# Kernel tuning notes

Hardware: AMD Instinct MI355X
Metric: run time of the kernel (lower is better)

The kernel has to match this reference:

```python
import jax, jax.numpy as jnp
import numpy as np

N = 30000        # nodes
E_EDGES = 960000 # edges (avg degree 32)
G = 16           # graphs in batch
D_IN, D_H, D_OUT = 6, 256, 256
L = 3            # GraphConv layers per expert
N_EXP, TOP_K = 8, 2


def _lin(key, fan_in, shape):
    return jax.random.normal(key, shape, dtype=jnp.float32) / np.sqrt(fan_in)


def setup_inputs() -> dict:
    key = jax.random.key(0)
    ks = jax.random.split(key, 12)
    x = jax.random.normal(ks[0], (N, D_IN), dtype=jnp.float32)
    edge_index = jax.random.randint(ks[1], (2, E_EDGES), 0, N, dtype=jnp.int64)
    batch = jnp.sort(jax.random.randint(ks[2], (N,), 0, G, dtype=jnp.int64))
    return {
        "x": x,
        "edge_index": edge_index,
        "batch": batch,
        # SharedBusEncoder: Linear(in, hidden) + ReLU
        "enc_W": _lin(ks[3], D_IN, (D_IN, D_H)),
        "enc_b": jnp.zeros((D_H,), jnp.float32),
        # BaseRouter: Linear(hidden+2, hidden) -> ReLU -> Linear(hidden, n_experts)
        "r_W1": _lin(ks[4], D_H + 2, (D_H + 2, D_H)),
        "r_b1": jnp.zeros((D_H,), jnp.float32),
        "r_W2": _lin(ks[5], D_H, (D_H, N_EXP)),
        "r_b2": jnp.zeros((N_EXP,), jnp.float32),
        # GraphConvExpert: L layers of PyG GraphConv (lin_rel on aggregated
        # neighbors + lin_root on self), stacked over [layer, expert].
        "Wrel": _lin(ks[6], D_H, (L, N_EXP, D_H, D_OUT)),
        "brel": jnp.zeros((L, N_EXP, D_OUT), jnp.float32),
        "Wroot": _lin(ks[7], D_H, (L, N_EXP, D_H, D_OUT)),
    }


def _forward(x, edge_index, batch, enc_W, enc_b, r_W1, r_b1, r_W2, r_b2,
             Wrel, brel, Wroot):
    src, dst = edge_index[0], edge_index[1]
    # encoder
    h = jax.nn.relu(x @ enc_W + enc_b)  # [N, D_H]

    # graph size features: per-node [log(#nodes), log(#edges)] of its graph
    n_g = jax.ops.segment_sum(jnp.ones((N,), jnp.float32), batch, num_segments=G)
    e_g = jax.ops.segment_sum(jnp.ones((E_EDGES,), jnp.float32), batch[src], num_segments=G)
    size = jnp.log(jnp.maximum(jnp.stack([n_g, e_g], axis=-1), 1.0))  # [G, 2]
    size_feat = size[batch]  # [N, 2]

    # router + sparse top-k routing
    r_h = jax.nn.relu(jnp.concatenate([h, size_feat], axis=-1) @ r_W1 + r_b1)
    logits = r_h @ r_W2 + r_b2            # [N, E]
    probs = jax.nn.softmax(logits, axis=-1)
    vals, idx = jax.lax.top_k(probs, TOP_K)
    vals = vals / jnp.sum(vals, axis=-1, keepdims=True)
    sparse = jnp.zeros((N, N_EXP), probs.dtype).at[
        jnp.arange(N)[:, None], idx].set(vals)  # [N, E]

    # all-expert GraphConv stacks (dense over experts, as in the original)
    agg0 = jax.ops.segment_sum(h[src], dst, num_segments=N)  # [N, D_H]
    H = jnp.einsum('nd,edf->enf', agg0, Wrel[0]) + brel[0][:, None, :] \
        + jnp.einsum('nd,edf->enf', h, Wroot[0])             # [E, N, D]
    for l in range(1, L):
        H = jax.nn.relu(H)
        A = jax.vmap(lambda hh: jax.ops.segment_sum(hh[src], dst, num_segments=N))(H)
        H = jnp.einsum('end,edf->enf', A, Wrel[l]) + brel[l][:, None, :] \
            + jnp.einsum('end,edf->enf', H, Wroot[l])

    # mask-and-sum combine
    return jnp.einsum('enf,ne->nf', H, sparse)  # [N, D_OUT]


def reference(x, edge_index, batch, enc_W, enc_b, r_W1, r_b1, r_W2, r_b2,
              Wrel, brel, Wroot):
    return _forward(x, edge_index, batch, enc_W, enc_b, r_W1, r_b1, r_W2,
                    r_b2, Wrel, brel, Wroot)
```

## Files before the change

kernel.cpp:

```cpp
#include <hip/hip_runtime.h>
#include <hip/hip_bf16.h>
#include <math.h>

#define NEXP 8
#define GNUM 16
#define DH 256

typedef __attribute__((ext_vector_type(8))) short s16x8;
typedef __attribute__((ext_vector_type(4))) float f32x4;
typedef unsigned short u16;
typedef unsigned int u32;

__device__ __forceinline__ float bitsToF(u32 b){ union{u32 u; float f;} c; c.u=b; return c.f; }
__device__ __forceinline__ u16 f2bf(float f){
  union{float f; u32 u;} c; c.f=f;
  u32 r = c.u + 0x7fffu + ((c.u>>16)&1u);
  return (u16)(r>>16);
}

#define GLOAD_LDS16(gp, lp) __builtin_amdgcn_global_load_lds( \
    (const __attribute__((address_space(1))) unsigned int*)(gp), \
    (__attribute__((address_space(3))) unsigned int*)(lp), 16, 0, 0)

__global__ void count_edges_k(const int* __restrict__ ei, const int* __restrict__ batch,
                              int* __restrict__ deg, int* __restrict__ eg, int E){
  __shared__ int leg[GNUM];
  int t = threadIdx.x;
  if (t < GNUM) leg[t] = 0;
  __syncthreads();
  int i = blockIdx.x*blockDim.x + t;
  if (i < E){
    int s = ei[i];
    int d = ei[E + i];
    atomicAdd(&deg[d], 1);
    atomicAdd(&leg[batch[s]], 1);
  }
  __syncthreads();
  if (t < GNUM){ int v = leg[t]; if (v) atomicAdd(&eg[t], v); }
}

__global__ void count_nodes_k(const int* __restrict__ batch, int* __restrict__ ng, int N){
  __shared__ int lng[GNUM];
  int t = threadIdx.x;
  if (t < GNUM) lng[t] = 0;
  __syncthreads();
  int i = blockIdx.x*blockDim.x + t;
  if (i < N) atomicAdd(&lng[batch[i]], 1);
  __syncthreads();
  if (t < GNUM){ int v = lng[t]; if (v) atomicAdd(&ng[t], v); }
}

#define SCAN_T 1024
#define SCAN_CH 32
__global__ __launch_bounds__(1024) void scan_deg_k(const int* __restrict__ deg,
    int* __restrict__ row_ptr, int* __restrict__ cursor, int N){
  __shared__ int part[SCAN_T];
  int t = threadIdx.x;
  int base = t*SCAN_CH;
  int loc[SCAN_CH];
  int s = 0;
  #pragma unroll
  for (int j=0;j<SCAN_CH;j++){
    int i = base+j;
    int v = (i<N)? deg[i] : 0;
    loc[j] = s; s += v;
  }
  part[t] = s;
  __syncthreads();
  for (int off=1; off<SCAN_T; off<<=1){
    int add = (t>=off)? part[t-off] : 0;
    __syncthreads();
    part[t] += add;
    __syncthreads();
  }
  int ex = (t==0)? 0 : part[t-1];
  #pragma unroll
  for (int j=0;j<SCAN_CH;j++){
    int i = base+j;
    if (i<N){ int v = ex + loc[j]; row_ptr[i]=v; cursor[i]=v; }
  }
  if (t == SCAN_T-1) row_ptr[N] = part[SCAN_T-1];
}

__global__ void scatter_edges_k(const int* __restrict__ ei, int* __restrict__ cursor,
                                int* __restrict__ csr_src, int E){
  int i = blockIdx.x*blockDim.x + threadIdx.x;
  if (i>=E) return;
  int s = ei[i];
  int d = ei[E + i];
  int pos = atomicAdd(&cursor[d], 1);
  csr_src[pos] = s;
}

__global__ void size_feats_k(const int* __restrict__ ng, const int* __restrict__ eg,
                             float* __restrict__ sizef){
  int g = threadIdx.x;
  if (g < GNUM){
    sizef[g*2]   = logf(fmaxf((float)ng[g], 1.f));
    sizef[g*2+1] = logf(fmaxf((float)eg[g], 1.f));
  }
}

__global__ void mark_fail_k(float* out){ out[0] = __builtin_nanf(""); }

__global__ __launch_bounds__(256) void encoder_k(const float* __restrict__ x,
    const float* __restrict__ W, const float* __restrict__ b,
    float* __restrict__ hf, u16* __restrict__ bh, int N){
  int n = blockIdx.x; if (n>=N) return;
  int f = threadIdx.x;
  float acc = b[f];
  #pragma unroll
  for (int k=0;k<6;k++) acc += x[n*6+k]*W[k*DH+f];
  acc = fmaxf(acc, 0.f);
  hf[(size_t)n*DH+f] = acc;
  bh[(size_t)n*DH+f] = f2bf(acc);
}

__global__ __launch_bounds__(256) void convw_k(const float* __restrict__ Wrel,
    const float* __restrict__ Wroot, u16* __restrict__ WT){
  __shared__ float tile[64][65];
  int tx = threadIdx.x;
  int ty = threadIdx.y;
  int kt = blockIdx.x & 3, ct = blockIdx.x >> 2;
  int srcRoot = blockIdx.y;
  int le = blockIdx.z;
  const float* src = (srcRoot ? Wroot : Wrel) + (size_t)le*65536;
  #pragma unroll
  for (int i=0;i<16;i++){
    int kl = ty + i*4;
    tile[kl][tx] = src[(size_t)(kt*64 + kl)*256 + ct*64 + tx];
  }
  __syncthreads();
  u16* dst = WT + (size_t)le*131072 + (srcRoot ? 256 : 0) + kt*64;
  #pragma unroll
  for (int i=0;i<16;i++){
    int cl = ty + i*4;
    dst[(size_t)(ct*64 + cl)*512 + tx] = f2bf(tile[tx][cl]);
  }
}

#define R1N 32
__global__ __launch_bounds__(256) void router1_k(
    const float* __restrict__ hf, const float* __restrict__ sizef,
    const int* __restrict__ batch,
    const float* __restrict__ W1, const float* __restrict__ b1,
    float* __restrict__ rh, int N)
{
  __shared__ float xin[R1N][264];
  int t = threadIdx.x;
  int lane = t & 63, w = t >> 6;
  int n0 = blockIdx.x * R1N;
  #pragma unroll
  for (int i=0;i<R1N;i++){
    int n = n0 + i;
    xin[i][t] = (n<N) ? hf[(size_t)n*DH + t] : 0.f;
  }
  if (t < R1N){
    int n = n0 + t;
    int g = (n<N) ? (int)batch[n] : 0;
    xin[t][256] = sizef[g*2];
    xin[t][257] = sizef[g*2+1];
    xin[t][258] = 0.f; xin[t][259] = 0.f;
    xin[t][260] = 0.f; xin[t][261] = 0.f; xin[t][262] = 0.f; xin[t][263] = 0.f;
  }
  __syncthreads();

  int wn = w*8;
  float bb[4];
  #pragma unroll
  for (int c=0;c<4;c++) bb[c] = b1[lane + c*64];
  float acc[8][4];
  #pragma unroll
  for (int i=0;i<8;i++)
    #pragma unroll
    for (int c=0;c<4;c++) acc[i][c] = bb[c];

  #pragma unroll 2
  for (int k4=0; k4<256; k4+=4){
    float w4[4][4];
    #pragma unroll
    for (int j=0;j<4;j++)
      #pragma unroll
      for (int c=0;c<4;c++)
        w4[j][c] = W1[(size_t)(k4+j)*DH + lane + c*64];
    #pragma unroll
    for (int i=0;i<8;i++){
      f32x4 xv = *(const f32x4*)&xin[wn+i][k4];
      #pragma unroll
      for (int j=0;j<4;j++)
        #pragma unroll
        for (int c=0;c<4;c++)
          acc[i][c] += xv[j]*w4[j][c];
    }
  }
  float w256[4], w257[4];
  #pragma unroll
  for (int c=0;c<4;c++){
    w256[c] = W1[(size_t)256*DH + lane + c*64];
    w257[c] = W1[(size_t)257*DH + lane + c*64];
  }
  #pragma unroll
  for (int i=0;i<8;i++){
    float s0 = xin[wn+i][256], s1 = xin[wn+i][257];
    #pragma unroll
    for (int c=0;c<4;c++) acc[i][c] += s0*w256[c] + s1*w257[c];
  }
  #pragma unroll
  for (int i=0;i<8;i++){
    int n = n0 + wn + i;
    if (n < N){
      #pragma unroll
      for (int c=0;c<4;c++)
        rh[(size_t)n*DH + lane + c*64] = fmaxf(acc[i][c], 0.f);
    }
  }
}

__global__ __launch_bounds__(256) void router2_k(
    const float* __restrict__ rh, const float* __restrict__ W2,
    const float* __restrict__ b2,
    int* __restrict__ ridx, float* __restrict__ rval, int N)
{
  __shared__ float w2s[NEXP][260];
  int t = threadIdx.x;
  for (int i=t; i<NEXP*DH; i+=256){
    int e = i >> 8, k = i & 255;
    w2s[e][k] = W2[(size_t)k*NEXP + e];
  }
  __syncthreads();
  int lane = t & 63, w = t >> 6;
  int n = blockIdx.x*4 + w;
  if (n >= N) return;
  const float* r = rh + (size_t)n*DH;
  float p[NEXP];
  #pragma unroll
  for (int e=0;e<NEXP;e++) p[e] = 0.f;
  #pragma unroll
  for (int c=0;c<4;c++){
    int k = lane + c*64;
    float rv = r[k];
    #pragma unroll
    for (int e=0;e<NEXP;e++) p[e] += rv * w2s[e][k];
  }
  #pragma unroll
  for (int off=1; off<64; off<<=1){
    #pragma unroll
    for (int e=0;e<NEXP;e++) p[e] += __shfl_xor(p[e], off, 64);
  }
  if (lane == 0){
    float l0[NEXP];
    #pragma unroll
    for (int e=0;e<NEXP;e++) l0[e] = p[e] + b2[e];
    float m = l0[0];
    #pragma unroll
    for (int e=1;e<NEXP;e++) m = fmaxf(m, l0[e]);
    float ex[NEXP];
    #pragma unroll
    for (int e=0;e<NEXP;e++) ex[e] = expf(l0[e]-m);
    int e0=0; float b0v=ex[0];
    #pragma unroll
    for (int e=1;e<NEXP;e++) if (ex[e]>b0v){b0v=ex[e]; e0=e;}
    int e1=(e0==0)?1:0; float b1v=ex[e1];
    #pragma unroll
    for (int e=0;e<NEXP;e++) if (e!=e0 && ex[e]>b1v){b1v=ex[e]; e1=e;}
    float sv = b0v + b1v;
    rval[n*2]   = b0v/sv;
    rval[n*2+1] = b1v/sv;
    ridx[n*2]   = e0;
    ridx[n*2+1] = e1;
  }
}

__global__ __launch_bounds__(256) void rsort_k(const int* __restrict__ ridx,
    int* __restrict__ cnt, int* __restrict__ plist, int* __restrict__ ppos, int N){
  __shared__ int lcnt[NEXP];
  __shared__ int lbase[NEXP];
  int t = threadIdx.x;
  int n = blockIdx.x*256 + t;
  if (t < NEXP) lcnt[t] = 0;
  __syncthreads();
  int e0=0, e1=0, o0=0, o1=0;
  if (n < N){
    e0 = ridx[n*2];
    e1 = ridx[n*2+1];
    o0 = atomicAdd(&lcnt[e0], 1);
    o1 = atomicAdd(&lcnt[e1], 1);
  }
  __syncthreads();
  if (t < NEXP) lbase[t] = atomicAdd(&cnt[t], lcnt[t]);
  __syncthreads();
  if (n < N){
    int p0 = lbase[e0] + o0;
    int p1 = lbase[e1] + o1;
    plist[(size_t)e0*N + p0] = n;
    plist[(size_t)e1*N + p1] = n;
    ppos[n*2]   = p0;
    ppos[n*2+1] = p1;
  }
}

__device__ __forceinline__ void agg_row(const u16* __restrict__ H,
    u16* __restrict__ Arow, const int* __restrict__ row_ptr,
    const int* __restrict__ csr_src, int node, int lane){
  int beg = row_ptr[node], end = row_ptr[node+1];
  float a0=0.f,a1=0.f,a2=0.f,a3=0.f;
  const u16* Hl = H + (lane<<2);
  int i = beg;
  for (; i+8<=end; i+=8){
    int sarr[8];
    #pragma unroll
    for (int u=0;u<8;u++) sarr[u] = csr_src[i+u];
    #pragma unroll
    for (int u=0;u<8;u++){
      uint2 v = *(const uint2*)(Hl + ((size_t)sarr[u]<<8));
      a0 += bitsToF(v.x<<16);
      a1 += bitsToF(v.x & 0xffff0000u);
      a2 += bitsToF(v.y<<16);
      a3 += bitsToF(v.y & 0xffff0000u);
    }
  }
  for (; i<end; ++i){
    int s = csr_src[i];
    uint2 v = *(const uint2*)(Hl + ((size_t)s<<8));
    a0 += bitsToF(v.x<<16);
    a1 += bitsToF(v.x & 0xffff0000u);
    a2 += bitsToF(v.y<<16);
    a3 += bitsToF(v.y & 0xffff0000u);
  }
  uint2 o;
  o.x = ((u32)f2bf(a1)<<16) | f2bf(a0);
  o.y = ((u32)f2bf(a3)<<16) | f2bf(a2);
  *(uint2*)(Arow + (lane<<2)) = o;
}

__global__ __launch_bounds__(256) void agg0_k(const u16* __restrict__ H,
    u16* __restrict__ A, const int* __restrict__ row_ptr,
    const int* __restrict__ csr_src, int N){
  int node = blockIdx.x*4 + (threadIdx.x>>6);
  if (node >= N) return;
  int lane = threadIdx.x & 63;
  agg_row(H, A + ((size_t)node<<8), row_ptr, csr_src, node, lane);
}

__device__ __forceinline__ void agg1_body(const u16* __restrict__ Hsrc,
    u16* __restrict__ Aout, const int* __restrict__ row_ptr,
    const int* __restrict__ csr_src, int N, int base, int cntN,
    int ezMask, int ezShift){
  int bid = blockIdx.x;
  int el = bid & ezMask;
  int xb = bid >> ezShift;
  int node = base + xb*4 + (threadIdx.x>>6);
  if (node >= base + cntN) return;
  int lane = threadIdx.x & 63;
  size_t NS = (size_t)N*DH;
  agg_row(Hsrc + (size_t)el*NS, Aout + (size_t)el*NS + ((size_t)node<<8),
          row_ptr, csr_src, node, lane);
}
__global__ __launch_bounds__(256) void agg1a_k(const u16* __restrict__ Hsrc,
    u16* __restrict__ Aout, const int* __restrict__ row_ptr,
    const int* __restrict__ csr_src, int N, int base, int cntN,
    int ezMask, int ezShift){
  agg1_body(Hsrc, Aout, row_ptr, csr_src, N, base, cntN, ezMask, ezShift);
}
__global__ __launch_bounds__(256) void agg1b_k(const u16* __restrict__ Hsrc,
    u16* __restrict__ Aout, const int* __restrict__ row_ptr,
    const int* __restrict__ csr_src, int N, int base, int cntN,
    int ezMask, int ezShift){
  agg1_body(Hsrc, Aout, row_ptr, csr_src, N, base, cntN, ezMask, ezShift);
}

__global__ __launch_bounds__(256) void agg2sg_k(const u16* __restrict__ Hsrc,
    u16* __restrict__ Aout, u16* __restrict__ Rout,
    const int* __restrict__ row_ptr, const int* __restrict__ csr_src,
    const int* __restrict__ plist, const int* __restrict__ cnt,
    int N, int gBase){
  int el = blockIdx.y;
  int idx = blockIdx.x*4 + (threadIdx.x>>6);
  if (idx >= cnt[gBase + el]) return;
  int node = plist[(size_t)(gBase + el)*N + idx];
  size_t NS = (size_t)N*DH;
  const u16* H = Hsrc + (size_t)el*NS;
  int lane = threadIdx.x & 63;
  uint2 rootv = *(const uint2*)(H + ((size_t)node<<8) + (lane<<2));
  agg_row(H, Aout + (size_t)el*NS + ((size_t)idx<<8), row_ptr, csr_src, node, lane);
  *(uint2*)(Rout + (size_t)el*NS + ((size_t)idx<<8) + (lane<<2)) = rootv;
}

__device__ __forceinline__ void gemm_bk64_body(
    const u16* __restrict__ aBase, const u16* __restrict__ rBase,
    const u16* __restrict__ wBase, const float* __restrict__ be,
    u16* __restrict__ Oe, int N, int relu_flag, u16* As, u16* Bs)
{
  int tid = threadIdx.x;
  int lane = tid & 63, w = tid >> 6;
  int wr = w >> 1, wc = w & 1;
  int m0 = blockIdx.x * 128;
  int n0 = blockIdx.y * 128;

  int lr8 = lane >> 3;
  int p   = (lane & 7) ^ lr8;
  long long asrc[4]; u16* aL[4];
  long long bsrc[4]; u16* bL[4];
  #pragma unroll
  for (int j=0;j<4;j++){
    int c = w*4 + j;
    int arow = m0 + c*8 + lr8; if (arow >= N) arow = N-1;
    asrc[j] = (long long)arow*256 + p*8;
    aL[j] = As + (size_t)c*512;
    int bcol = n0 + c*8 + lr8;
    bsrc[j] = (long long)bcol*512 + p*8;
    bL[j] = Bs + (size_t)c*512;
  }

  f32x4 acc[4][4];
  #pragma unroll
  for (int a=0;a<4;a++)
    #pragma unroll
    for (int b=0;b<4;b++) acc[a][b] = (f32x4){0.f,0.f,0.f,0.f};

  int fr = lane & 15;
  int fkq = lane >> 4;

  #pragma unroll 1
  for (int kk=0; kk<8; ++kk){
    const u16* sA = (kk < 4) ? aBase : rBase;
    int koff = (kk & 3) * 64;
    #pragma unroll
    for (int j=0;j<4;j++){
      GLOAD_LDS16(sA + asrc[j] + koff, aL[j]);
      GLOAD_LDS16(wBase + bsrc[j] + kk*64, bL[j]);
    }
    __syncthreads();
    #pragma unroll
    for (int kin=0; kin<2; ++kin){
      unsigned fb = (unsigned)(fkq*16 + kin*64);
      s16x8 af[4], bf[4];
      #pragma unroll
      for (int mi=0;mi<4;mi++){
        int row = wr*64 + mi*16 + fr;
        unsigned byte = ((unsigned)row << 7) + (fb ^ (((unsigned)(row & 7)) << 4));
        af[mi] = *(const s16x8*)((const char*)As + byte);
      }
      #pragma unroll
      for (int ni=0;ni<4;ni++){
        int col = wc*64 + ni*16 + fr;
        unsigned byte = ((unsigned)col << 7) + (fb ^ (((unsigned)(col & 7)) << 4));
        bf[ni] = *(const s16x8*)((const char*)Bs + byte);
      }
      #pragma unroll
      for (int mi=0;mi<4;mi++)
        #pragma unroll
        for (int ni=0;ni<4;ni++)
          acc[mi][ni] = __builtin_amdgcn_mfma_f32_16x16x32_bf16(af[mi], bf[ni], acc[mi][ni], 0, 0, 0);
    }
    __syncthreads();
  }

  int fq = lane >> 4;
  #pragma unroll
  for (int ni=0;ni<4;ni++){
    int col = n0 + wc*64 + ni*16 + fr;
    float bv = be[col];
    #pragma unroll
    for (int mi=0;mi<4;mi++){
      int rowb = m0 + wr*64 + mi*16 + fq*4;
      f32x4 v = acc[mi][ni];
      #pragma unroll
      for (int j=0;j<4;j++){
        int row = rowb + j;
        if (row < N){
          float o = v[j] + bv;
          if (relu_flag) o = fmaxf(o, 0.f);
          Oe[(size_t)row*DH + col] = f2bf(o);
        }
      }
    }
  }
}

__global__ __launch_bounds__(256,2) void gemm0g_k(
    const u16* __restrict__ A0, const u16* __restrict__ bh,
    const u16* __restrict__ WT, const float* __restrict__ bias,
    u16* __restrict__ Hout, int N){
  __shared__ u16 As[128*64];
  __shared__ u16 Bs[128*64];
  int el = blockIdx.z;
  gemm_bk64_body(A0, bh, WT + (size_t)el*(256*512), bias + el*256,
                 Hout + (size_t)el*((size_t)N*DH), N, 1, As, Bs);
}
__global__ __launch_bounds__(256,2) void gemm1g_k(
    const u16* __restrict__ Aagg, const u16* __restrict__ Hroot,
    const u16* __restrict__ WT, const float* __restrict__ bias,
    u16* __restrict__ Hout, int N){
  __shared__ u16 As[128*64];
  __shared__ u16 Bs[128*64];
  int el = blockIdx.z;
  size_t NS = (size_t)N*DH;
  gemm_bk64_body(Aagg + (size_t)el*NS, Hroot + (size_t)el*NS,
                 WT + (size_t)el*(256*512), bias + el*256,
                 Hout + (size_t)el*NS, N, 1, As, Bs);
}

__global__ __launch_bounds__(256,2) void gemm2sg_k(
    const u16* __restrict__ Aagg, const u16* __restrict__ Rc,
    const u16* __restrict__ WT, const float* __restrict__ bias,
    u16* __restrict__ Hout, const int* __restrict__ cnte, int N, int gBase)
{
  __shared__ u16 As[128*32];
  __shared__ u16 Bs[128*32];
  int el = blockIdx.z;
  int cnt = cnte[gBase + el];
  int m0 = blockIdx.x * 128;
  if (m0 >= cnt) return;
  size_t NS = (size_t)N*DH;
  const u16* aBase = Aagg + (size_t)el*NS;
  const u16* rBase = Rc + (size_t)el*NS;
  const u16* wBase = WT + (size_t)el*(256*512);
  const float* be  = bias + el*256;
  u16* Oe = Hout + (size_t)el*NS;

  int tid = threadIdx.x;
  int lane = tid & 63, w = tid >> 6;
  int wr = w >> 1, wc = w & 1;
  int n0 = blockIdx.y * 128;

  int lrow = lane >> 2;
  int q8   = (((lane & 3) ^ ((lane >> 3) & 3))) * 8;
  int r0 = w*16 + lrow;
  int r1 = (w+4)*16 + lrow;
  int ai0 = m0 + r0; if (ai0 >= cnt) ai0 = cnt-1;
  int ai1 = m0 + r1; if (ai1 >= cnt) ai1 = cnt-1;
  long long aoff0 = (long long)ai0*256 + q8;
  long long aoff1 = (long long)ai1*256 + q8;
  long long boff0 = (long long)(n0 + r0)*512 + q8;
  long long boff1 = (long long)(n0 + r1)*512 + q8;
  u16* aL0 = As + (size_t)w*512;
  u16* aL1 = As + (size_t)(w+4)*512;
  u16* bL0 = Bs + (size_t)w*512;
  u16* bL1 = Bs + (size_t)(w+4)*512;

  f32x4 acc[4][4];
  #pragma unroll
  for (int a=0;a<4;a++)
    #pragma unroll
    for (int b=0;b<4;b++) acc[a][b] = (f32x4){0.f,0.f,0.f,0.f};

  int fr = lane & 15;
  int fk = (((lane >> 4) ^ ((fr >> 1) & 3))) * 8;
  const u16* aRead = As + (size_t)(wr*64 + fr)*32 + fk;
  const u16* bRead = Bs + (size_t)(wc*64 + fr)*32 + fk;

  #pragma unroll 1
  for (int half=0; half<2; ++half){
    const u16* sA = half ? rBase : aBase;
    #pragma unroll 1
    for (int kk=0; kk<8; ++kk){
      int kin = kk*32;
      int kg  = half*256 + kin;
      GLOAD_LDS16(sA + aoff0 + kin, aL0);
      GLOAD_LDS16(sA + aoff1 + kin, aL1);
      GLOAD_LDS16(wBase + boff0 + kg, bL0);
      GLOAD_LDS16(wBase + boff1 + kg, bL1);
      __syncthreads();
      s16x8 af[4], bf[4];
      #pragma unroll
      for (int mi=0;mi<4;mi++) af[mi] = *(const s16x8*)(aRead + mi*16*32);
      #pragma unroll
      for (int ni=0;ni<4;ni++) bf[ni] = *(const s16x8*)(bRead + ni*16*32);
      #pragma unroll
      for (int mi=0;mi<4;mi++)
        #pragma unroll
        for (int ni=0;ni<4;ni++)
          acc[mi][ni] = __builtin_amdgcn_mfma_f32_16x16x32_bf16(af[mi], bf[ni], acc[mi][ni], 0, 0, 0);
      __syncthreads();
    }
  }
  int fq = lane >> 4;
  #pragma unroll
  for (int ni=0;ni<4;ni++){
    int col = n0 + wc*64 + ni*16 + fr;
    float bv = be[col];
    #pragma unroll
    for (int mi=0;mi<4;mi++){
      int rowb = m0 + wr*64 + mi*16 + fq*4;
      f32x4 v = acc[mi][ni];
      #pragma unroll
      for (int j=0;j<4;j++){
        int row = rowb + j;
        if (row < cnt){
          float o = v[j] + bv;
          Oe[(size_t)row*DH + col] = f2bf(o);
        }
      }
    }
  }
}

__global__ __launch_bounds__(256) void combine_spg_k(const u16* __restrict__ H3c,
    const int* __restrict__ ridx, const int* __restrict__ ppos,
    const float* __restrict__ rval, float* __restrict__ out,
    int N, int gBase, int ezCnt, int first){
  int n = blockIdx.x; if (n>=N) return;
  int f = threadIdx.x;
  size_t NS = (size_t)N*DH;
  size_t off = (size_t)n*DH + f;
  float acc = first ? 0.f : out[off];
  #pragma unroll
  for (int p=0;p<2;p++){
    int el = ridx[n*2+p] - gBase;
    if (el >= 0 && el < ezCnt)
      acc += rval[n*2+p] * bitsToF(((u32)H3c[(size_t)el*NS + (size_t)ppos[n*2+p]*DH + f])<<16);
  }
  out[off] = acc;
}

extern "C" void kernel_launch(void* const* d_in, const int* in_sizes, int n_in,
                              void* d_out, int out_size, void* d_ws, size_t ws_size,
                              hipStream_t stream)
{
  const float* x    = (const float*)d_in[0];
  const int*   ei   = (const int*)d_in[1];
  const int*   batch= (const int*)d_in[2];
  const float* encW = (const float*)d_in[3];
  const float* encb = (const float*)d_in[4];
  const float* rW1  = (const float*)d_in[5];
  const float* rb1  = (const float*)d_in[6];
  const float* rW2  = (const float*)d_in[7];
  const float* rb2  = (const float*)d_in[8];
  const float* Wrel = (const float*)d_in[9];
  const float* brel = (const float*)d_in[10];
  const float* Wroot= (const float*)d_in[11];
  int N = in_sizes[2];
  int E = in_sizes[1]/2;
  float* out = (float*)d_out;
  (void)n_in; (void)out_size;

  size_t NS = (size_t)N*DH;
  char* p = (char*)d_ws;
  auto carve = [&](size_t bytes)->char*{
    char* r = p; p += (bytes + 255) & ~(size_t)255; return r;
  };
  u16*  bh   = (u16*)carve(NS*2);
  u16*  WT   = (u16*)carve((size_t)3*NEXP*256*512*2);
  int*  deg  = (int*)carve((size_t)N*4 + 64*4);
  int*  ng   = deg + N;
  int*  eg   = ng + GNUM;
  int*  row_ptr = (int*)carve(((size_t)N+1)*4);
  int*  cursor  = (int*)carve((size_t)N*4);
  int*  csr     = (int*)carve((size_t)E*4);
  float* sizef  = (float*)carve(GNUM*2*4);
  int*  ridx    = (int*)carve((size_t)N*2*4);
  float* rvalv  = (float*)carve((size_t)N*2*4);
  int*  ecnt    = (int*)carve(NEXP*4);
  int*  plist   = (int*)carve((size_t)NEXP*N*4);
  int*  ppos    = (int*)carve((size_t)N*2*4);
  u16*  A0      = (u16*)carve(NS*2);
  size_t baseUsed = (size_t)(p - (char*)d_ws);

  int EZ = 0;
  for (int cand = NEXP; cand >= 1; cand >>= 1){
    if (baseUsed + (size_t)cand*3*NS*2 <= ws_size){ EZ = cand; break; }
  }
  if (EZ == 0){ mark_fail_k<<<1,1,0,stream>>>(out); return; }
  int ezShift = (EZ==8)?3 : (EZ==4)?2 : (EZ==2)?1 : 0;

  u16* Abuf = (u16*)carve((size_t)EZ*NS*2);
  u16* Hc   = (u16*)carve((size_t)EZ*NS*2);
  u16* Hn   = (u16*)carve((size_t)EZ*NS*2);
  float* hf; float* rh;
  if (EZ >= 2){ hf = (float*)Abuf; rh = (float*)Hn; }
  else {
    hf = (float*)carve(NS*4);
    rh = (float*)carve(NS*4);
    if ((size_t)(p - (char*)d_ws) > ws_size){ mark_fail_k<<<1,1,0,stream>>>(out); return; }
  }

  hipMemsetAsync(deg, 0, (size_t)N*4 + (size_t)2*GNUM*4, stream);
  hipMemsetAsync(ecnt, 0, NEXP*4, stream);

  int eb = (E + 255)/256;
  count_edges_k<<<eb, 256, 0, stream>>>(ei, batch, deg, eg, E);
  count_nodes_k<<<(N+255)/256, 256, 0, stream>>>(batch, ng, N);
  scan_deg_k<<<1, SCAN_T, 0, stream>>>(deg, row_ptr, cursor, N);
  scatter_edges_k<<<eb, 256, 0, stream>>>(ei, cursor, csr, E);
  size_feats_k<<<1, 64, 0, stream>>>(ng, eg, sizef);
  encoder_k<<<N, 256, 0, stream>>>(x, encW, encb, hf, bh, N);
  convw_k<<<dim3(16,2,3*NEXP), dim3(64,4), 0, stream>>>(Wrel, Wroot, WT);
  router1_k<<<(N+R1N-1)/R1N, 256, 0, stream>>>(hf, sizef, batch, rW1, rb1, rh, N);
  router2_k<<<(N+3)/4, 256, 0, stream>>>(rh, rW2, rb2, ridx, rvalv, N);
  rsort_k<<<(N+255)/256, 256, 0, stream>>>(ridx, ecnt, plist, ppos, N);

  int aggx = (N+3)/4;
  int mt128 = (N+127)/128;
  const size_t WE = (size_t)256*512;

  agg0_k<<<aggx, 256, 0, stream>>>(bh, A0, row_ptr, csr, N);

  int half0 = (((N+1)/2) + 3) & ~3;
  if (half0 > N) half0 = N;
  int half1 = N - half0;
  int g1a = ((half0+3)/4)*EZ;
  int g1b = ((half1+3)/4)*EZ;

  for (int g = 0; g < NEXP; g += EZ){
    gemm0g_k<<<dim3(mt128,2,EZ), 256, 0, stream>>>(A0, bh,
        WT + ((size_t)0*NEXP + g)*WE, brel + (0*NEXP + g)*256, Hc, N);
    agg1a_k<<<g1a, 256, 0, stream>>>(Hc, Abuf, row_ptr, csr, N, 0, half0, EZ-1, ezShift);
    if (half1 > 0)
      agg1b_k<<<g1b, 256, 0, stream>>>(Hc, Abuf, row_ptr, csr, N, half0, half1, EZ-1, ezShift);
    gemm1g_k<<<dim3(mt128,2,EZ), 256, 0, stream>>>(Abuf, Hc,
        WT + ((size_t)1*NEXP + g)*WE, brel + (1*NEXP + g)*256, Hn, N);
    agg2sg_k<<<dim3(aggx,EZ), 256, 0, stream>>>(Hn, Abuf, Hc, row_ptr, csr,
        plist, ecnt, N, g);
    gemm2sg_k<<<dim3(mt128,2,EZ), 256, 0, stream>>>(Abuf, Hc,
        WT + ((size_t)2*NEXP + g)*WE, brel + (2*NEXP + g)*256, Hn, ecnt, N, g);
    combine_spg_k<<<N, 256, 0, stream>>>(Hn, ridx, ppos, rvalv, out, N, g, EZ, g==0);
  }
}
```

Baseline: 1.295 ms.

## Interleave layer-0 expert outputs per node so the first aggregation gathers contiguous rows

The layer-0 GEMM now writes its output interleaved as [node, expert, feature] instead of expert-major. The first-layer aggregation becomes a single kernel with one block per node and one wave per expert. Each neighbour's data for all experts is therefore one contiguous chunk, and the CSR indices are read once and shared across experts. The GEMM body gains row-stride parameters so layer 0 can write, and layer 1 can read, the strided root operand, at the cost of strided stores and loads in those GEMMs and larger blocks (up to 512 threads) in the aggregation.

```diff
diff --git a/kernel.cpp b/kernel.cpp
--- a/kernel.cpp
+++ b/kernel.cpp
@@ -342,31 +342,44 @@
   agg_row(H, A + ((size_t)node<<8), row_ptr, csr_src, node, lane);
 }
 
-__device__ __forceinline__ void agg1_body(const u16* __restrict__ Hsrc,
+__global__ void agg1i_k(const u16* __restrict__ Hi,
     u16* __restrict__ Aout, const int* __restrict__ row_ptr,
-    const int* __restrict__ csr_src, int N, int base, int cntN,
-    int ezMask, int ezShift){
-  int bid = blockIdx.x;
-  int el = bid & ezMask;
-  int xb = bid >> ezShift;
-  int node = base + xb*4 + (threadIdx.x>>6);
-  if (node >= base + cntN) return;
+    const int* __restrict__ csr_src, int N, int EZ){
+  int node = blockIdx.x;
+  if (node >= N) return;
+  int el = threadIdx.x >> 6;
   int lane = threadIdx.x & 63;
   size_t NS = (size_t)N*DH;
-  agg_row(Hsrc + (size_t)el*NS, Aout + (size_t)el*NS + ((size_t)node<<8),
-          row_ptr, csr_src, node, lane);
-}
-__global__ __launch_bounds__(256) void agg1a_k(const u16* __restrict__ Hsrc,
-    u16* __restrict__ Aout, const int* __restrict__ row_ptr,
-    const int* __restrict__ csr_src, int N, int base, int cntN,
-    int ezMask, int ezShift){
-  agg1_body(Hsrc, Aout, row_ptr, csr_src, N, base, cntN, ezMask, ezShift);
-}
-__global__ __launch_bounds__(256) void agg1b_k(const u16* __restrict__ Hsrc,
-    u16* __restrict__ Aout, const int* __restrict__ row_ptr,
-    const int* __restrict__ csr_src, int N, int base, int cntN,
-    int ezMask, int ezShift){
-  agg1_body(Hsrc, Aout, row_ptr, csr_src, N, base, cntN, ezMask, ezShift);
+  const u16* Hl = Hi + (size_t)el*DH + (lane<<2);
+  int beg = row_ptr[node], end = row_ptr[node+1];
+  float a0=0.f,a1=0.f,a2=0.f,a3=0.f;
+  int strideSh = (EZ==8)?11 : (EZ==4)?10 : (EZ==2)?9 : 8;
+  int i = beg;
+  for (; i+8<=end; i+=8){
+    int sarr[8];
+    #pragma unroll
+    for (int u=0;u<8;u++) sarr[u] = csr_src[i+u];
+    #pragma unroll
+    for (int u=0;u<8;u++){
+      uint2 v = *(const uint2*)(Hl + ((size_t)sarr[u]<<strideSh));
+      a0 += bitsToF(v.x<<16);
+      a1 += bitsToF(v.x & 0xffff0000u);
+      a2 += bitsToF(v.y<<16);
+      a3 += bitsToF(v.y & 0xffff0000u);
+    }
+  }
+  for (; i<end; ++i){
+    int s = csr_src[i];
+    uint2 v = *(const uint2*)(Hl + ((size_t)s<<strideSh));
+    a0 += bitsToF(v.x<<16);
+    a1 += bitsToF(v.x & 0xffff0000u);
+    a2 += bitsToF(v.y<<16);
+    a3 += bitsToF(v.y & 0xffff0000u);
+  }
+  uint2 o;
+  o.x = ((u32)f2bf(a1)<<16) | f2bf(a0);
+  o.y = ((u32)f2bf(a3)<<16) | f2bf(a2);
+  *(uint2*)(Aout + (size_t)el*NS + ((size_t)node<<8) + (lane<<2)) = o;
 }
 
 __global__ __launch_bounds__(256) void agg2sg_k(const u16* __restrict__ Hsrc,
@@ -388,8 +401,10 @@
 
 __device__ __forceinline__ void gemm_bk64_body(
     const u16* __restrict__ aBase, const u16* __restrict__ rBase,
+    long long rstrideElems,
     const u16* __restrict__ wBase, const float* __restrict__ be,
-    u16* __restrict__ Oe, int N, int relu_flag, u16* As, u16* Bs)
+    u16* __restrict__ Oe, long long ostrideElems,
+    int N, int relu_flag, u16* As, u16* Bs)
 {
   int tid = threadIdx.x;
   int lane = tid & 63, w = tid >> 6;
@@ -399,13 +414,14 @@
 
   int lr8 = lane >> 3;
   int p   = (lane & 7) ^ lr8;
-  long long asrc[4]; u16* aL[4];
+  long long asrc[4]; long long rsrc[4]; u16* aL[4];
   long long bsrc[4]; u16* bL[4];
   #pragma unroll
   for (int j=0;j<4;j++){
     int c = w*4 + j;
     int arow = m0 + c*8 + lr8; if (arow >= N) arow = N-1;
     asrc[j] = (long long)arow*256 + p*8;
+    rsrc[j] = (long long)arow*rstrideElems + p*8;
     aL[j] = As + (size_t)c*512;
     int bcol = n0 + c*8 + lr8;
     bsrc[j] = (long long)bcol*512 + p*8;
@@ -423,11 +439,12 @@
 
   #pragma unroll 1
   for (int kk=0; kk<8; ++kk){
-    const u16* sA = (kk < 4) ? aBase : rBase;
+    int useRoot = (kk >= 4);
     int koff = (kk & 3) * 64;
     #pragma unroll
     for (int j=0;j<4;j++){
-      GLOAD_LDS16(sA + asrc[j] + koff, aL[j]);
+      if (useRoot) GLOAD_LDS16(rBase + rsrc[j] + koff, aL[j]);
+      else         GLOAD_LDS16(aBase + asrc[j] + koff, aL[j]);
       GLOAD_LDS16(wBase + bsrc[j] + kk*64, bL[j]);
     }
     __syncthreads();
@@ -471,7 +488,7 @@
         if (row < N){
           float o = v[j] + bv;
           if (relu_flag) o = fmaxf(o, 0.f);
-          Oe[(size_t)row*DH + col] = f2bf(o);
+          Oe[(size_t)row*ostrideElems + col] = f2bf(o);
         }
       }
     }
@@ -481,24 +498,25 @@
 __global__ __launch_bounds__(256,2) void gemm0g_k(
     const u16* __restrict__ A0, const u16* __restrict__ bh,
     const u16* __restrict__ WT, const float* __restrict__ bias,
-    u16* __restrict__ Hout, int N){
+    u16* __restrict__ Hi, int N, int EZ){
   __shared__ u16 As[128*64];
   __shared__ u16 Bs[128*64];
   int el = blockIdx.z;
-  gemm_bk64_body(A0, bh, WT + (size_t)el*(256*512), bias + el*256,
-                 Hout + (size_t)el*((size_t)N*DH), N, 1, As, Bs);
+  gemm_bk64_body(A0, bh, 256,
+                 WT + (size_t)el*(256*512), bias + el*256,
+                 Hi + (size_t)el*DH, (long long)EZ*DH, N, 1, As, Bs);
 }
 __global__ __launch_bounds__(256,2) void gemm1g_k(
-    const u16* __restrict__ Aagg, const u16* __restrict__ Hroot,
+    const u16* __restrict__ Aagg, const u16* __restrict__ Hi,
     const u16* __restrict__ WT, const float* __restrict__ bias,
-    u16* __restrict__ Hout, int N){
+    u16* __restrict__ Hout, int N, int EZ){
   __shared__ u16 As[128*64];
   __shared__ u16 Bs[128*64];
   int el = blockIdx.z;
   size_t NS = (size_t)N*DH;
-  gemm_bk64_body(Aagg + (size_t)el*NS, Hroot + (size_t)el*NS,
+  gemm_bk64_body(Aagg + (size_t)el*NS, Hi + (size_t)el*DH, (long long)EZ*DH,
                  WT + (size_t)el*(256*512), bias + el*256,
-                 Hout + (size_t)el*NS, N, 1, As, Bs);
+                 Hout + (size_t)el*NS, 256, N, 1, As, Bs);
 }
 
 __global__ __launch_bounds__(256,2) void gemm2sg_k(
@@ -662,7 +680,6 @@
     if (baseUsed + (size_t)cand*3*NS*2 <= ws_size){ EZ = cand; break; }
   }
   if (EZ == 0){ mark_fail_k<<<1,1,0,stream>>>(out); return; }
-  int ezShift = (EZ==8)?3 : (EZ==4)?2 : (EZ==2)?1 : 0;
 
   u16* Abuf = (u16*)carve((size_t)EZ*NS*2);
   u16* Hc   = (u16*)carve((size_t)EZ*NS*2);
@@ -696,20 +713,12 @@
 
   agg0_k<<<aggx, 256, 0, stream>>>(bh, A0, row_ptr, csr, N);
 
-  int half0 = (((N+1)/2) + 3) & ~3;
-  if (half0 > N) half0 = N;
-  int half1 = N - half0;
-  int g1a = ((half0+3)/4)*EZ;
-  int g1b = ((half1+3)/4)*EZ;
-
   for (int g = 0; g < NEXP; g += EZ){
     gemm0g_k<<<dim3(mt128,2,EZ), 256, 0, stream>>>(A0, bh,
-        WT + ((size_t)0*NEXP + g)*WE, brel + (0*NEXP + g)*256, Hc, N);
-    agg1a_k<<<g1a, 256, 0, stream>>>(Hc, Abuf, row_ptr, csr, N, 0, half0, EZ-1, ezShift);
-    if (half1 > 0)
-      agg1b_k<<<g1b, 256, 0, stream>>>(Hc, Abuf, row_ptr, csr, N, half0, half1, EZ-1, ezShift);
+        WT + ((size_t)0*NEXP + g)*WE, brel + (0*NEXP + g)*256, Hc, N, EZ);
+    agg1i_k<<<N, 64*EZ, 0, stream>>>(Hc, Abuf, row_ptr, csr, N, EZ);
     gemm1g_k<<<dim3(mt128,2,EZ), 256, 0, stream>>>(Abuf, Hc,
-        WT + ((size_t)1*NEXP + g)*WE, brel + (1*NEXP + g)*256, Hn, N);
+        WT + ((size_t)1*NEXP + g)*WE, brel + (1*NEXP + g)*256, Hn, N, EZ);
     agg2sg_k<<<dim3(aggx,EZ), 256, 0, stream>>>(Hn, Abuf, Hc, row_ptr, csr,
         plist, ecnt, N, g);
     gemm2sg_k<<<dim3(mt128,2,EZ), 256, 0, stream>>>(Abuf, Hc,
```

New measurement: 1.385 ms. 6.9% more time.

## Split neighbor aggregation into feature-quarter passes with 4-way edge parallelism

Applied to the files above, without the earlier changes.

The layer-1 and layer-2 aggregation kernels now process one 64-column quarter of the 256-wide feature row per launch, running four launches in turn. Within a wave, 16 lanes cover the quarter's columns and 4 lane groups take different edges, then combine through cross-lane shuffles. The aim is to shrink the gathered working set per pass so it stays in cache, and to put more independent gathers in flight per wave. In exchange there are four times as many launches, the CSR indices are re-read once per quarter, and shuffle reductions are added; the agg1 two-half split is removed.

```diff
diff --git a/kernel.cpp b/kernel.cpp
--- a/kernel.cpp
+++ b/kernel.cpp
@@ -342,48 +342,90 @@
   agg_row(H, A + ((size_t)node<<8), row_ptr, csr_src, node, lane);
 }
 
-__device__ __forceinline__ void agg1_body(const u16* __restrict__ Hsrc,
+
+__global__ __launch_bounds__(256) void agg1q_k(const u16* __restrict__ Hsrc,
     u16* __restrict__ Aout, const int* __restrict__ row_ptr,
-    const int* __restrict__ csr_src, int N, int base, int cntN,
-    int ezMask, int ezShift){
+    const int* __restrict__ csr_src, int N, int qoff, int ezMask, int ezShift){
   int bid = blockIdx.x;
   int el = bid & ezMask;
   int xb = bid >> ezShift;
-  int node = base + xb*4 + (threadIdx.x>>6);
-  if (node >= base + cntN) return;
+  int node = xb*4 + (threadIdx.x>>6);
+  if (node >= N) return;
   int lane = threadIdx.x & 63;
+  int e4 = lane >> 4, c16 = lane & 15;
   size_t NS = (size_t)N*DH;
-  agg_row(Hsrc + (size_t)el*NS, Aout + (size_t)el*NS + ((size_t)node<<8),
-          row_ptr, csr_src, node, lane);
-}
-__global__ __launch_bounds__(256) void agg1a_k(const u16* __restrict__ Hsrc,
-    u16* __restrict__ Aout, const int* __restrict__ row_ptr,
-    const int* __restrict__ csr_src, int N, int base, int cntN,
-    int ezMask, int ezShift){
-  agg1_body(Hsrc, Aout, row_ptr, csr_src, N, base, cntN, ezMask, ezShift);
-}
-__global__ __launch_bounds__(256) void agg1b_k(const u16* __restrict__ Hsrc,
-    u16* __restrict__ Aout, const int* __restrict__ row_ptr,
-    const int* __restrict__ csr_src, int N, int base, int cntN,
-    int ezMask, int ezShift){
-  agg1_body(Hsrc, Aout, row_ptr, csr_src, N, base, cntN, ezMask, ezShift);
-}
-
-__global__ __launch_bounds__(256) void agg2sg_k(const u16* __restrict__ Hsrc,
+  const u16* Hq = Hsrc + (size_t)el*NS + qoff + (c16<<2);
+  int beg = row_ptr[node], end = row_ptr[node+1];
+  float a0=0.f,a1=0.f,a2=0.f,a3=0.f;
+  for (int i = beg; i < end; i += 4){
+    int ii = i + e4;
+    if (ii < end){
+      int s = csr_src[ii];
+      uint2 v = *(const uint2*)(Hq + ((size_t)s<<8));
+      a0 += bitsToF(v.x<<16);
+      a1 += bitsToF(v.x & 0xffff0000u);
+      a2 += bitsToF(v.y<<16);
+      a3 += bitsToF(v.y & 0xffff0000u);
+    }
+  }
+  #pragma unroll
+  for (int off=16; off<64; off<<=1){
+    a0 += __shfl_xor(a0, off, 64);
+    a1 += __shfl_xor(a1, off, 64);
+    a2 += __shfl_xor(a2, off, 64);
+    a3 += __shfl_xor(a3, off, 64);
+  }
+  if (e4 == 0){
+    uint2 o;
+    o.x = ((u32)f2bf(a1)<<16) | f2bf(a0);
+    o.y = ((u32)f2bf(a3)<<16) | f2bf(a2);
+    *(uint2*)(Aout + (size_t)el*NS + ((size_t)node<<8) + qoff + (c16<<2)) = o;
+  }
+}
+
+__global__ __launch_bounds__(256) void agg2q_k(const u16* __restrict__ Hsrc,
     u16* __restrict__ Aout, u16* __restrict__ Rout,
     const int* __restrict__ row_ptr, const int* __restrict__ csr_src,
     const int* __restrict__ plist, const int* __restrict__ cnt,
-    int N, int gBase){
-  int el = blockIdx.y;
-  int idx = blockIdx.x*4 + (threadIdx.x>>6);
+    int N, int gBase, int qoff, int ezMask, int ezShift){
+  int bid = blockIdx.x;
+  int el = bid & ezMask;
+  int xb = bid >> ezShift;
+  int idx = xb*4 + (threadIdx.x>>6);
   if (idx >= cnt[gBase + el]) return;
   int node = plist[(size_t)(gBase + el)*N + idx];
+  int lane = threadIdx.x & 63;
+  int e4 = lane >> 4, c16 = lane & 15;
   size_t NS = (size_t)N*DH;
-  const u16* H = Hsrc + (size_t)el*NS;
-  int lane = threadIdx.x & 63;
-  uint2 rootv = *(const uint2*)(H + ((size_t)node<<8) + (lane<<2));
-  agg_row(H, Aout + (size_t)el*NS + ((size_t)idx<<8), row_ptr, csr_src, node, lane);
-  *(uint2*)(Rout + (size_t)el*NS + ((size_t)idx<<8) + (lane<<2)) = rootv;
+  const u16* Hq = Hsrc + (size_t)el*NS + qoff + (c16<<2);
+  int beg = row_ptr[node], end = row_ptr[node+1];
+  float a0=0.f,a1=0.f,a2=0.f,a3=0.f;
+  for (int i = beg; i < end; i += 4){
+    int ii = i + e4;
+    if (ii < end){
+      int s = csr_src[ii];
+      uint2 v = *(const uint2*)(Hq + ((size_t)s<<8));
+      a0 += bitsToF(v.x<<16);
+      a1 += bitsToF(v.x & 0xffff0000u);
+      a2 += bitsToF(v.y<<16);
+      a3 += bitsToF(v.y & 0xffff0000u);
+    }
+  }
+  #pragma unroll
+  for (int off=16; off<64; off<<=1){
+    a0 += __shfl_xor(a0, off, 64);
+    a1 += __shfl_xor(a1, off, 64);
+    a2 += __shfl_xor(a2, off, 64);
+    a3 += __shfl_xor(a3, off, 64);
+  }
+  if (e4 == 0){
+    uint2 rv = *(const uint2*)(Hq + ((size_t)node<<8));
+    uint2 o;
+    o.x = ((u32)f2bf(a1)<<16) | f2bf(a0);
+    o.y = ((u32)f2bf(a3)<<16) | f2bf(a2);
+    *(uint2*)(Aout + (size_t)el*NS + ((size_t)idx<<8) + qoff + (c16<<2)) = o;
+    *(uint2*)(Rout + (size_t)el*NS + ((size_t)idx<<8) + qoff + (c16<<2)) = rv;
+  }
 }
 
 __device__ __forceinline__ void gemm_bk64_body(
@@ -696,22 +738,18 @@
 
   agg0_k<<<aggx, 256, 0, stream>>>(bh, A0, row_ptr, csr, N);
 
-  int half0 = (((N+1)/2) + 3) & ~3;
-  if (half0 > N) half0 = N;
-  int half1 = N - half0;
-  int g1a = ((half0+3)/4)*EZ;
-  int g1b = ((half1+3)/4)*EZ;
+  int gq = aggx*EZ;
 
   for (int g = 0; g < NEXP; g += EZ){
     gemm0g_k<<<dim3(mt128,2,EZ), 256, 0, stream>>>(A0, bh,
         WT + ((size_t)0*NEXP + g)*WE, brel + (0*NEXP + g)*256, Hc, N);
-    agg1a_k<<<g1a, 256, 0, stream>>>(Hc, Abuf, row_ptr, csr, N, 0, half0, EZ-1, ezShift);
-    if (half1 > 0)
-      agg1b_k<<<g1b, 256, 0, stream>>>(Hc, Abuf, row_ptr, csr, N, half0, half1, EZ-1, ezShift);
+    for (int q = 0; q < 4; ++q)
+      agg1q_k<<<gq, 256, 0, stream>>>(Hc, Abuf, row_ptr, csr, N, q*64, EZ-1, ezShift);
     gemm1g_k<<<dim3(mt128,2,EZ), 256, 0, stream>>>(Abuf, Hc,
         WT + ((size_t)1*NEXP + g)*WE, brel + (1*NEXP + g)*256, Hn, N);
-    agg2sg_k<<<dim3(aggx,EZ), 256, 0, stream>>>(Hn, Abuf, Hc, row_ptr, csr,
-        plist, ecnt, N, g);
+    for (int q = 0; q < 4; ++q)
+      agg2q_k<<<gq, 256, 0, stream>>>(Hn, Abuf, Hc, row_ptr, csr,
+          plist, ecnt, N, g, q*64, EZ-1, ezShift);
     gemm2sg_k<<<dim3(mt128,2,EZ), 256, 0, stream>>>(Abuf, Hc,
         WT + ((size_t)2*NEXP + g)*WE, brel + (2*NEXP + g)*256, Hn, ecnt, N, g);
     combine_spg_k<<<N, 256, 0, stream>>>(Hn, ridx, ppos, rvalv, out, N, g, EZ, g==0);
```

Measured after the change: 2.185 ms. +68.7%, slower.
